# Kernel optimization log

Hardware: AMD Instinct MI355X
Metric: run time of the kernel (lower is better)

The kernel has to match this reference:

```python
import jax, jax.numpy as jnp
import numpy as np

NUM_AGENT = 200
LOOK_BACK = 10
NUM_CTRL = 9
DIM = 512
HEADS = 8
DIM_HEAD = 64
N = NUM_AGENT * LOOK_BACK + NUM_CTRL  # 2009
BATCH = 4
SCALE = DIM_HEAD ** -0.5


def _build_mask():
    # eye(num_agent) repeat_interleaved by look_back on rows and cols == kron with ones(lb,lb)
    m = jnp.kron(jnp.eye(NUM_AGENT, dtype=jnp.float32),
                 jnp.ones((LOOK_BACK, LOOK_BACK), jnp.float32))
    # pad with zeros for the control-feature rows/cols
    return jnp.pad(m, ((0, NUM_CTRL), (0, NUM_CTRL)))  # [N, N]


def _split_heads(t):
    b, n, hd = t.shape
    return t.reshape(b, n, HEADS, hd // HEADS).transpose(0, 2, 1, 3)  # [b,h,n,d]


def setup_inputs() -> dict:
    key = jax.random.key(0)
    ks = jax.random.split(key, 5)
    inner = HEADS * DIM_HEAD
    return {
        "x": jax.random.normal(ks[0], (BATCH, N, DIM), jnp.float32),
        "w_qkv": jax.random.normal(ks[1], (DIM, inner * 3), jnp.float32) * 0.02,
        "w_qk_self": jax.random.normal(ks[2], (DIM, inner * 2), jnp.float32) * 0.02,
        "w_out": jax.random.normal(ks[3], (inner, DIM), jnp.float32) * 0.02,
        "b_out": jnp.zeros((DIM,), jnp.float32),
    }


def reference(x, w_qkv, w_qk_self, w_out, b_out):
    mask = _build_mask()  # [N, N], broadcasts over [b, h]
    q, k, v = map(_split_heads, jnp.split(x @ w_qkv, 3, axis=-1))
    q_s, k_s = map(_split_heads, jnp.split(x @ w_qk_self, 2, axis=-1))
    dots = jnp.einsum('bhnd,bhmd->bhnm', q, k) * SCALE
    dots_self = jnp.einsum('bhnd,bhmd->bhnm', q_s, k_s) * SCALE
    blended = mask * dots_self + (1.0 - mask) * dots
    attn = jax.nn.softmax(blended, axis=-1)  # [b,h,n,n]
    out = jnp.einsum('bhnm,bhmd->bhnd', attn, v)
    out = out.transpose(0, 2, 1, 3).reshape(x.shape[0], N, HEADS * DIM_HEAD)
    return out @ w_out + b_out, attn
```

## Files before the change

kernel.cpp:

```cpp
#include <hip/hip_runtime.h>
#include <hip/hip_bf16.h>


#define N_TOK   2009
#define NPAD    2048
#define NTILES  16
#define NT2     32
#define BATCH_  4
#define HEADS_  8
#define MROWS   8036
#define SCALE_  0.125f
#define RPB_A   256
#define RPV     128
#define PFP     68

typedef __attribute__((ext_vector_type(8)))  short sh8;
typedef __attribute__((ext_vector_type(16))) float f32x16;

static inline int cdiv(int a, int b) { return (a + b - 1) / b; }

__device__ __forceinline__ float4 ld4(const float* p) {
    return *reinterpret_cast<const float4*>(p);
}
__device__ __forceinline__ unsigned short f2bf(float f) {
    __hip_bfloat16 h = __float2bfloat16(f);
    return *reinterpret_cast<unsigned short*>(&h);
}
__device__ __forceinline__ float bf2f(unsigned short u) {
    return __uint_as_float(((unsigned)u) << 16);
}
__device__ __forceinline__ void cvt8(const float4& a, const float4& b, sh8& hi, sh8& lo) {
    float f[8] = {a.x, a.y, a.z, a.w, b.x, b.y, b.z, b.w};
#pragma unroll
    for (int i = 0; i < 8; ++i) {
        unsigned short h = f2bf(f[i]);
        hi[i] = (short)h;
        lo[i] = (short)f2bf(f[i] - bf2f(h));
    }
}
__device__ __forceinline__ void cvt8p(const float4& a, const float4& b, sh8& hi) {
#pragma unroll
    for (int i = 0; i < 4; ++i) {
        hi[i]     = (short)f2bf((&a.x)[i]);
        hi[4 + i] = (short)f2bf((&b.x)[i]);
    }
}
typedef const __attribute__((address_space(1))) void gas_void;
typedef __attribute__((address_space(3))) void las_void;
__device__ __forceinline__ void gll16(const void* g, void* l) {
    __builtin_amdgcn_global_load_lds((gas_void*)g, (las_void*)l, 16, 0, 0);
}

__global__ __launch_bounds__(256)
void convert_x(const float* __restrict__ x, unsigned short* __restrict__ xh,
               unsigned short* __restrict__ xl)
{
    const int mt = blockIdx.x;
    const int w  = threadIdx.x >> 6;
    const int kc = threadIdx.x & 63;
    for (int it = 0; it < 8; ++it) {
        int rg = it * 4 + w;
        sh8 hi[4], lo[4];
#pragma unroll
        for (int rr = 0; rr < 4; ++rr) {
            int row = rg * 4 + rr;
            int gm = mt * 128 + row;
            int b = gm >> 11, gr = gm & 2047;
            float4 a = make_float4(0.f, 0.f, 0.f, 0.f), c = a;
            if (gr < N_TOK) {
                const float* p = x + ((size_t)b * N_TOK + gr) * 512 + kc * 8;
                a = ld4(p); c = ld4(p + 4);
            }
            cvt8(a, c, hi[rr], lo[rr]);
        }
        size_t base = ((size_t)(mt * 64 + kc) * 128 + rg * 4) * 8;
#pragma unroll
        for (int rr = 0; rr < 4; ++rr) {
            *reinterpret_cast<sh8*>(xh + base + rr * 8) = hi[rr];
            *reinterpret_cast<sh8*>(xl + base + rr * 8) = lo[rr];
        }
    }
}

__global__ __launch_bounds__(256)
void convert_w(const float* __restrict__ wqkv, const float* __restrict__ wself,
               const float* __restrict__ wout,
               unsigned short* __restrict__ qh, unsigned short* __restrict__ ql,
               unsigned short* __restrict__ sh, unsigned short* __restrict__ sl,
               unsigned short* __restrict__ oh, unsigned short* __restrict__ ol)
{
    int cid = blockIdx.x * 256 + threadIdx.x;
    int nt_all = cid >> 13, rem = cid & 8191;
    int kc = rem >> 7, col = rem & 127;
    const float* src; unsigned short *dh, *dl; int Nn, ntl;
    if (nt_all < 12)      { src = wqkv;  dh = qh; dl = ql; Nn = 1536; ntl = nt_all; }
    else if (nt_all < 20) { src = wself; dh = sh; dl = sl; Nn = 1024; ntl = nt_all - 12; }
    else                  { src = wout;  dh = oh; dl = ol; Nn = 512;  ntl = nt_all - 20; }
    float f[8];
#pragma unroll
    for (int i = 0; i < 8; ++i)
        f[i] = src[(size_t)(kc * 8 + i) * Nn + ntl * 128 + col];
    sh8 hi, lo;
    cvt8(make_float4(f[0], f[1], f[2], f[3]), make_float4(f[4], f[5], f[6], f[7]), hi, lo);
    size_t off = ((size_t)(ntl * 64 + kc) * 128 + col) * 8;
    *reinterpret_cast<sh8*>(dh + off) = hi;
    *reinterpret_cast<sh8*>(dl + off) = lo;
}

template<int MODE>
__global__ __launch_bounds__(512)
void gemm_bf16(const unsigned short* __restrict__ Ah, const unsigned short* __restrict__ Al,
               const unsigned short* __restrict__ Bh, const unsigned short* __restrict__ Bl,
               float* __restrict__ C, const float* __restrict__ bias)
{
    __shared__ __align__(16) unsigned short AhS[2][4096], AlS[2][4096],
                                            BhS[2][4096], BlS[2][4096];
    const int tid = threadIdx.x, lane = tid & 63, wid = tid >> 6;
    const int mt = blockIdx.x, ntile = blockIdx.y;
    const int wm = wid >> 2, wn = wid & 3;
    const int lj = lane & 31, g = lane >> 5;

    const unsigned short* Asrc_h = Ah + (size_t)mt * 65536;
    const unsigned short* Asrc_l = Al + (size_t)mt * 65536;
    const unsigned short* Bsrc_h = Bh + (size_t)ntile * 65536;
    const unsigned short* Bsrc_l = Bl + (size_t)ntile * 65536;

#define GSTAGE(BUF, S) do {                                                      \
    gll16(Asrc_h + (size_t)(S) * 4096 + tid * 8, (char*)AhS[BUF] + tid * 16);    \
    gll16(Asrc_l + (size_t)(S) * 4096 + tid * 8, (char*)AlS[BUF] + tid * 16);    \
    gll16(Bsrc_h + (size_t)(S) * 4096 + tid * 8, (char*)BhS[BUF] + tid * 16);    \
    gll16(Bsrc_l + (size_t)(S) * 4096 + tid * 8, (char*)BlS[BUF] + tid * 16);    \
} while (0)

    f32x16 acc[2];
#pragma unroll
    for (int i = 0; i < 16; ++i) { acc[0][i] = 0.f; acc[1][i] = 0.f; }

    GSTAGE(0, 0);
    for (int s = 0; s < 16; ++s) {
        const int buf = s & 1;
        __syncthreads();
        if (s + 1 < 16) GSTAGE(buf ^ 1, s + 1);
#pragma unroll
        for (int ks = 0; ks < 2; ++ks) {
            const int kcl = 2 * ks + g;
            sh8 bh = *reinterpret_cast<const sh8*>(BhS[buf] + (kcl * 128 + wn * 32 + lj) * 8);
            sh8 bl = *reinterpret_cast<const sh8*>(BlS[buf] + (kcl * 128 + wn * 32 + lj) * 8);
#pragma unroll
            for (int Mt = 0; Mt < 2; ++Mt) {
                sh8 ah = *reinterpret_cast<const sh8*>(AhS[buf] + (kcl * 128 + wm * 64 + Mt * 32 + lj) * 8);
                sh8 al = *reinterpret_cast<const sh8*>(AlS[buf] + (kcl * 128 + wm * 64 + Mt * 32 + lj) * 8);
                acc[Mt] = __builtin_amdgcn_mfma_f32_32x32x16_bf16(ah, bh, acc[Mt], 0, 0, 0);
                acc[Mt] = __builtin_amdgcn_mfma_f32_32x32x16_bf16(ah, bl, acc[Mt], 0, 0, 0);
                acc[Mt] = __builtin_amdgcn_mfma_f32_32x32x16_bf16(al, bh, acc[Mt], 0, 0, 0);
            }
        }
    }
#undef GSTAGE

#pragma unroll
    for (int Mt = 0; Mt < 2; ++Mt) {
#pragma unroll
        for (int reg = 0; reg < 16; ++reg) {
            int rloc = wm * 64 + Mt * 32 + (reg & 3) + 8 * (reg >> 2) + 4 * g;
            int gm = mt * 128 + rloc;
            int b = gm >> 11, gr = gm & 2047;
            if (gr < N_TOK) {
                int coln = ntile * 128 + wn * 32 + lj;
                float v = acc[Mt][reg];
                size_t idx;
                if (MODE == 1)
                    idx = ((size_t)(coln >> 9) * MROWS + (size_t)b * N_TOK + gr) * 512 + (coln & 511);
                else if (MODE == 0)
                    idx = ((size_t)b * N_TOK + gr) * 1024 + coln;
                else {
                    v += bias[coln];
                    idx = ((size_t)b * N_TOK + gr) * 512 + coln;
                }
                C[idx] = v;
            }
        }
    }
}

__global__ __launch_bounds__(256)
void selfE_k(const float* __restrict__ proj2, float* __restrict__ selfE)
{
    __shared__ float qs[10][64];
    __shared__ float ks[10][68];
    const int a = blockIdx.x;
    const int h = blockIdx.y & 7;
    const int b = blockIdx.y >> 3;
    const size_t rowbase = (size_t)b * N_TOK + a * 10;

    for (int i = threadIdx.x; i < 320; i += 256) {
        int r = i >> 4;
        int c = (i & 15) * 4;
        const float* src = proj2 + (rowbase + (r % 10)) * 1024
                         + (r < 10 ? 0 : 512) + h * 64 + c;
        float4 v = ld4(src);
        if (r < 10) *reinterpret_cast<float4*>(&qs[r][c]) = v;
        else        *reinterpret_cast<float4*>(&ks[r - 10][c]) = v;
    }
    __syncthreads();
    if (threadIdx.x < 100) {
        int r = threadIdx.x / 10, c = threadIdx.x % 10;
        float acc = 0.f;
#pragma unroll 8
        for (int d = 0; d < 64; ++d) acc += qs[r][d] * ks[c][d];
        int bh = b * HEADS_ + h;
        selfE[((size_t)bh * 2000 + a * 10 + r) * 10 + c] = __expf(acc * SCALE_);
    }
}

__global__ __launch_bounds__(256)
void convert_kv(const float* __restrict__ Kf, const float* __restrict__ Vf,
                unsigned short* __restrict__ Khg, unsigned short* __restrict__ Klg,
                unsigned short* __restrict__ Vtg)
{
    __shared__ float vtile[128][66];
    const int t  = blockIdx.x;
    const int h  = blockIdx.y & 7;
    const int b  = blockIdx.y >> 3;
    const int bh = blockIdx.y;
    const size_t bN = (size_t)b * N_TOK;
    const size_t tbase = ((size_t)bh * NTILES + t) * 8192;
    const int tid = threadIdx.x;

    {
        int r = tid >> 1, q = tid & 1;
        int gj = t * 128 + r;
        float4 f[8];
        if (gj < N_TOK) {
            const float* kp = Kf + (bN + gj) * 512 + h * 64 + q * 32;
#pragma unroll
            for (int i = 0; i < 8; ++i) f[i] = ld4(kp + 4 * i);
        } else {
#pragma unroll
            for (int i = 0; i < 8; ++i) f[i] = make_float4(0.f, 0.f, 0.f, 0.f);
        }
#pragma unroll
        for (int cp = 0; cp < 4; ++cp) {
            sh8 hi, lo;
            cvt8(f[2 * cp], f[2 * cp + 1], hi, lo);
            int kc = q * 4 + cp;
            size_t off = tbase + ((size_t)kc * 128 + r) * 8;
            *reinterpret_cast<sh8*>(Khg + off) = hi;
            *reinterpret_cast<sh8*>(Klg + off) = lo;
        }
    }
    {
        int r = tid >> 1, q = tid & 1;
        int gj = t * 128 + r;
        const float* vp = Vf + (bN + gj) * 512 + h * 64 + q * 32;
#pragma unroll
        for (int i = 0; i < 8; ++i) {
            float4 v = (gj < N_TOK) ? ld4(vp + 4 * i) : make_float4(0.f, 0.f, 0.f, 0.f);
            *reinterpret_cast<float4*>(&vtile[r][q * 32 + 4 * i]) = v;
        }
    }
    __syncthreads();
    {
        int d = tid & 63, jg = tid >> 6;
#pragma unroll
        for (int jj = 0; jj < 4; ++jj) {
            int jc = jg * 4 + jj;
            sh8 pk;
#pragma unroll
            for (int i = 0; i < 8; ++i) pk[i] = (short)f2bf(vtile[jc * 8 + i][d]);
            *reinterpret_cast<sh8*>(Vtg + tbase + ((size_t)jc * 64 + d) * 8) = pk;
        }
    }
}

__global__ __launch_bounds__(512, 2)
void attn_rowsum(const float* __restrict__ Qf,
                 const unsigned short* __restrict__ Khg,
                 const float* __restrict__ selfE,
                 float* __restrict__ rowinv)
{
    __shared__ __align__(16) unsigned short KhS[2][8192];
    __shared__ float selfS[RPB_A * 10];

    const int bid = blockIdx.x;
    const int xcd = bid & 7, idx = bid >> 3;
    const int bh  = xcd * 4 + (idx >> 3);
    const int bx  = idx & 7;
    const int h = bh & 7, b = bh >> 3;
    const int tid = threadIdx.x, lane = tid & 63, wid = tid >> 6;
    const int row0 = bx * RPB_A;
    const int wr = wid * 32;
    const size_t bN = (size_t)b * N_TOK;
    const int lj = lane & 31, g = lane >> 5;

    for (int i = tid; i < RPB_A * 10; i += 512) {
        int r = i / 10, c = i - r * 10;
        int gr = row0 + r;
        selfS[i] = (gr < 2000) ? selfE[((size_t)bh * 2000 + gr) * 10 + c] : 0.f;
    }

    sh8 qh[4];
    {
        int grow = row0 + wr + lj;
        bool val = grow < N_TOK;
        const float* qp = Qf + (bN + (val ? grow : 0)) * 512 + h * 64;
#pragma unroll
        for (int ks = 0; ks < 4; ++ks) {
            int kc = 2 * ks + g;
            float4 a = val ? ld4(qp + kc * 8)     : make_float4(0.f, 0.f, 0.f, 0.f);
            float4 c = val ? ld4(qp + kc * 8 + 4) : make_float4(0.f, 0.f, 0.f, 0.f);
            cvt8p(a, c, qh[ks]);
        }
    }

    const unsigned short* ktiles = Khg + (size_t)bh * NTILES * 8192;
#define RSTAGE(T) do {                                                          \
    const unsigned short* kt = ktiles + (size_t)(T) * 8192;                     \
    char* dst = (char*)KhS[(T) & 1];                                            \
    _Pragma("unroll") for (int i = 0; i < 2; ++i)                               \
        gll16(kt + i * 4096 + tid * 8, dst + i * 8192 + tid * 16); } while (0)

    RSTAGE(0);

    float rsacc[16];
#pragma unroll
    for (int i = 0; i < 16; ++i) rsacc[i] = 0.f;

    const int alo = (row0 / 10) * 10;
    const int rmax = row0 + RPB_A - 1 < 1999 ? row0 + RPB_A - 1 : 1999;
    const int ahi = (rmax / 10) * 10 + 10;

    for (int t = 0; t < NTILES; ++t) {
        __syncthreads();
        if (t + 1 < NTILES) RSTAGE(t + 1);
        const unsigned short* kb = KhS[t & 1];
        const bool dtile = (alo < t * 128 + 128) && (ahi > t * 128);
#pragma unroll
        for (int ct = 0; ct < 4; ++ct) {
            sh8 kf[4];
#pragma unroll
            for (int ks = 0; ks < 4; ++ks)
                kf[ks] = *reinterpret_cast<const sh8*>(kb + ((2 * ks + g) * 128 + 32 * ct + lj) * 8);
            f32x16 s;
#pragma unroll
            for (int i = 0; i < 16; ++i) s[i] = 0.f;
#pragma unroll
            for (int ks = 0; ks < 4; ++ks)
                s = __builtin_amdgcn_mfma_f32_32x32x16_bf16(qh[ks], kf[ks], s, 0, 0, 0);
            const int gj = t * 128 + 32 * ct + lj;
            if (gj < N_TOK) {
#pragma unroll
                for (int reg = 0; reg < 16; ++reg) {
                    int rloc = wr + (reg & 3) + 8 * (reg >> 2) + 4 * g;
                    int grow = row0 + rloc;
                    float e = __expf(s[reg] * SCALE_);
                    if (dtile && grow < 2000) {
                        int a0 = (grow / 10) * 10;
                        unsigned cc = (unsigned)(gj - a0);
                        if (cc < 10u) e = selfS[rloc * 10 + (int)cc];
                    }
                    rsacc[reg] += e;
                }
            }
        }
    }
#undef RSTAGE

#pragma unroll
    for (int reg = 0; reg < 16; ++reg) {
        float v = rsacc[reg];
        v += __shfl_xor(v, 1);  v += __shfl_xor(v, 2);
        v += __shfl_xor(v, 4);  v += __shfl_xor(v, 8);
        v += __shfl_xor(v, 16);
        rsacc[reg] = v;
    }
    if (lj == 0) {
#pragma unroll
        for (int reg = 0; reg < 16; ++reg) {
            int rloc = wr + (reg & 3) + 8 * (reg >> 2) + 4 * g;
            int grow = row0 + rloc;
            rowinv[(size_t)bh * NPAD + row0 + rloc] =
                (grow < N_TOK) ? 1.0f / rsacc[reg] : 0.f;
        }
    }
}

__global__ __launch_bounds__(512, 2)
void attn_pv(const float* __restrict__ Qf,
             const unsigned short* __restrict__ Khg,
             const unsigned short* __restrict__ Klg,
             const unsigned short* __restrict__ Vtg,
             const float* __restrict__ selfE,
             const float* __restrict__ rowinv,
             float* __restrict__ attn,
             unsigned short* __restrict__ Ohg, unsigned short* __restrict__ Olg)
{
    extern __shared__ __align__(16) char smem[];
    unsigned short* KhS = (unsigned short*)smem;
    unsigned short* KlS = KhS + 4096;
    unsigned short* VtS = KlS + 4096;
    float* Pf = (float*)(VtS + 8192);
    unsigned short* selfS = (unsigned short*)(Pf + RPV * PFP);
    float* rinvS = (float*)(selfS + RPV * 10);

    const int bid = blockIdx.x;
    const int xcd = bid & 7, idx = bid >> 3;
    const int bh  = xcd * 4 + (idx >> 4);
    const int bx  = idx & 15;
    const int h = bh & 7, b = bh >> 3;
    const int tid = threadIdx.x, lane = tid & 63, wid = tid >> 6;
    const int row0 = bx * RPV;
    const int wr = (wid & 3) * 32;
    const int cw = wid >> 2;
    const size_t bN = (size_t)b * N_TOK;
    const size_t abase = ((size_t)bh * N_TOK + row0) * N_TOK;
    const int lj = lane & 31, g = lane >> 5;

    for (int i = tid; i < RPV * 10; i += 512) {
        int r = i / 10, c = i - r * 10;
        int gr = row0 + r;
        selfS[i] = (gr < 2000) ? f2bf(selfE[((size_t)bh * 2000 + gr) * 10 + c]) : 0;
    }
    if (tid < RPV) rinvS[tid] = rowinv[(size_t)bh * NPAD + row0 + tid];

    sh8 qh[4], ql[4];
    {
        int grow = row0 + wr + lj;
        bool val = grow < N_TOK;
        const float* qp = Qf + (bN + (val ? grow : 0)) * 512 + h * 64;
#pragma unroll
        for (int ks = 0; ks < 4; ++ks) {
            int kc = 2 * ks + g;
            float4 a = val ? ld4(qp + kc * 8)     : make_float4(0.f, 0.f, 0.f, 0.f);
            float4 c = val ? ld4(qp + kc * 8 + 4) : make_float4(0.f, 0.f, 0.f, 0.f);
            cvt8(a, c, qh[ks], ql[ks]);
        }
    }

    const unsigned short* khT = Khg + (size_t)bh * NTILES * 8192;
    const unsigned short* klT = Klg + (size_t)bh * NTILES * 8192;
    const unsigned short* vtT = Vtg + (size_t)bh * NTILES * 8192;

#define STAGE_KH(T) gll16(khT + (size_t)((T) >> 1) * 8192                           \
        + ((size_t)(tid >> 6) * 128 + 64 * ((T) & 1) + (tid & 63)) * 8,             \
        (char*)KhS + tid * 16)
#define STAGE_KL(T) gll16(klT + (size_t)((T) >> 1) * 8192                           \
        + ((size_t)(tid >> 6) * 128 + 64 * ((T) & 1) + (tid & 63)) * 8,             \
        (char*)KlS + tid * 16)
#define STAGE_VT(T) gll16(vtT + (size_t)((T) >> 1) * 8192                           \
        + ((size_t)(8 * ((T) & 1) + (tid >> 6)) * 64 + (tid & 63)) * 8,             \
        (char*)(VtS + ((T) & 1) * 4096) + tid * 16)

    STAGE_KH(0); STAGE_KL(0); STAGE_VT(0);

    const int alo = (row0 / 10) * 10;
    const int rmax = row0 + RPV - 1 < 1999 ? row0 + RPV - 1 : 1999;
    const int ahi = (rmax / 10) * 10 + 10;

    f32x16 oacc;
#pragma unroll
    for (int i = 0; i < 16; ++i) oacc[i] = 0.f;

    __syncthreads();

    for (int t = 0; t < NT2; ++t) {
        const bool dtile = (alo < t * 64 + 64) && (ahi > t * 64);

        sh8 kfh[4], kfl[4];
#pragma unroll
        for (int ks = 0; ks < 4; ++ks) {
            int off = ((2 * ks + g) * 64 + 32 * cw + lj) * 8;
            kfh[ks] = *reinterpret_cast<const sh8*>(KhS + off);
            kfl[ks] = *reinterpret_cast<const sh8*>(KlS + off);
        }
        f32x16 s;
#pragma unroll
        for (int i = 0; i < 16; ++i) s[i] = 0.f;
#pragma unroll
        for (int ks = 0; ks < 4; ++ks) {
            s = __builtin_amdgcn_mfma_f32_32x32x16_bf16(qh[ks], kfh[ks], s, 0, 0, 0);
            s = __builtin_amdgcn_mfma_f32_32x32x16_bf16(qh[ks], kfl[ks], s, 0, 0, 0);
            s = __builtin_amdgcn_mfma_f32_32x32x16_bf16(ql[ks], kfh[ks], s, 0, 0, 0);
        }
        const int cin = 32 * cw + lj;
        const int gj  = t * 64 + cin;
        const bool jv = gj < N_TOK;
#pragma unroll
        for (int reg = 0; reg < 16; ++reg) {
            int rowl = (reg & 3) + 8 * (reg >> 2) + 4 * g;
            int rloc = wr + rowl;
            int grow = row0 + rloc;
            float e = 0.f;
            if (jv && grow < N_TOK) e = __expf(s[reg] * SCALE_);
            if (dtile && jv && grow < 2000) {
                int a0 = (grow / 10) * 10;
                unsigned cc = (unsigned)(gj - a0);
                if (cc < 10u) e = bf2f(selfS[rloc * 10 + (int)cc]);
            }
            Pf[rloc * PFP + cin] = e * rinvS[rloc];
        }
        __syncthreads();

        if (t + 1 < NT2) { STAGE_KH(t + 1); STAGE_KL(t + 1); STAGE_VT(t + 1); }
        const unsigned short* vtb = VtS + (t & 1) * 4096;
#pragma unroll
        for (int m = 0; m < 4; ++m) {
            const float* pp = &Pf[(wr + lj) * PFP + 16 * m + 8 * g];
            float4 a = ld4(pp), b4 = ld4(pp + 4);
            sh8 pa; cvt8p(a, b4, pa);
            sh8 vf = *reinterpret_cast<const sh8*>(vtb + ((2 * m + g) * 64 + 32 * cw + lj) * 8);
            oacc = __builtin_amdgcn_mfma_f32_32x32x16_bf16(pa, vf, oacc, 0, 0, 0);
        }
        {
            const int c4  = (tid & 15) * 4;
            const int gj0 = t * 64 + c4;
#pragma unroll
            for (int it = 0; it < 4; ++it) {
                int r = it * 32 + (tid >> 4);
                int grow = row0 + r;
                if (grow < N_TOK) {
                    float4 v = ld4(&Pf[r * PFP + c4]);
                    float* ap = attn + abase + (size_t)r * N_TOK + gj0;
                    if (gj0 + 3 < N_TOK) {
                        *reinterpret_cast<float4*>(ap) = v;
                    } else {
#pragma unroll
                        for (int e = 0; e < 4; ++e)
                            if (gj0 + e < N_TOK) ap[e] = (&v.x)[e];
                    }
                }
            }
        }
        __syncthreads();
    }
#undef STAGE_KH
#undef STAGE_KL
#undef STAGE_VT

    float* Ofull = (float*)smem;
#pragma unroll
    for (int reg = 0; reg < 16; ++reg) {
        int rloc = wr + (reg & 3) + 8 * (reg >> 2) + 4 * g;
        Ofull[rloc * 68 + 32 * cw + lj] = oacc[reg];
    }
    __syncthreads();
#pragma unroll
    for (int it = 0; it < 2; ++it) {
        int task = it * 512 + tid;
        int row = task >> 3, kq = task & 7;
        const float* op = Ofull + row * 68 + kq * 8;
        float4 a = ld4(op), c = ld4(op + 4);
        sh8 hi, lo; cvt8(a, c, hi, lo);
        int gm = b * 2048 + row0 + row;
        int mtile = gm >> 7, row128 = gm & 127;
        size_t off = ((size_t)(mtile * 64 + h * 8 + kq) * 128 + row128) * 8;
        *reinterpret_cast<sh8*>(Ohg + off) = hi;
        *reinterpret_cast<sh8*>(Olg + off) = lo;
    }
}

extern "C" void kernel_launch(void* const* d_in, const int* in_sizes, int n_in,
                              void* d_out, int out_size, void* d_ws, size_t ws_size,
                              hipStream_t stream)
{
    const float* x         = (const float*)d_in[0];
    const float* w_qkv     = (const float*)d_in[1];
    const float* w_qk_self = (const float*)d_in[2];
    const float* w_out     = (const float*)d_in[3];
    const float* b_out     = (const float*)d_in[4];

    float* out  = (float*)d_out;
    float* attn = out + (size_t)MROWS * 512;

    float* Qf = (float*)d_ws;
    float* Kf = Qf + (size_t)MROWS * 512;
    float* Vf = Kf + (size_t)MROWS * 512;
    float* p2 = Vf + (size_t)MROWS * 512;
    unsigned short* Khg = (unsigned short*)p2;
    unsigned short* Klg = Khg + 4194304;
    unsigned short* Vtg = Klg + 4194304;
    float* proj2 = p2;
    float* after_p2 = p2 + (size_t)MROWS * 1024;
    unsigned short* xh  = (unsigned short*)after_p2;
    unsigned short* xl  = xh + 4194304;
    unsigned short* Wqh = xl + 4194304;
    unsigned short* Wql = Wqh + 786432;
    unsigned short* Wsh = Wql + 786432;
    unsigned short* Wsl = Wsh + 524288;
    unsigned short* Woh = Wsl + 524288;
    unsigned short* Wol = Woh + 262144;
    float* rowinv = (float*)(Wol + 262144);
    float* selfE  = rowinv + 65536;
    unsigned short* Ohg = (unsigned short*)Kf;
    unsigned short* Olg = Ohg + 4194304;

    const int smem_pv = 8192 + 8192 + 16384
                      + RPV * PFP * 4
                      + RPV * 10 * 2 + RPV * 4;
    hipFuncSetAttribute((const void*)attn_pv,
                        hipFuncAttributeMaxDynamicSharedMemorySize, smem_pv);

    convert_x<<<64, 256, 0, stream>>>(x, xh, xl);
    convert_w<<<768, 256, 0, stream>>>(w_qkv, w_qk_self, w_out,
                                       Wqh, Wql, Wsh, Wsl, Woh, Wol);

    dim3 g1(64, 12);
    gemm_bf16<1><<<g1, 512, 0, stream>>>(xh, xl, Wqh, Wql, Qf, nullptr);

    dim3 g2(64, 8);
    gemm_bf16<0><<<g2, 512, 0, stream>>>(xh, xl, Wsh, Wsl, proj2, nullptr);

    dim3 gs(200, 32);
    selfE_k<<<gs, 256, 0, stream>>>(proj2, selfE);

    dim3 gc(NTILES, 32);
    convert_kv<<<gc, 256, 0, stream>>>(Kf, Vf, Khg, Klg, Vtg);

    attn_rowsum<<<256, 512, 0, stream>>>(Qf, Khg, selfE, rowinv);

    attn_pv<<<512, 512, smem_pv, stream>>>(Qf, Khg, Klg, Vtg, selfE, rowinv,
                                           attn, Ohg, Olg);

    dim3 g3(64, 4);
    gemm_bf16<2><<<g3, 512, 0, stream>>>(Ohg, Olg, Woh, Wol, out, b_out);
}
```

Baseline: 460.0 us.

## Relax attn_pv barriers so attention stores overlap the next tile's loads

Splits the attn_pv tile loop into QK and PV phase macros and peels off the last iteration. Each __syncthreads is replaced by a hand-written barrier: one waits only on LDS, and the other waits with vmcnt(4), so the four attention-row stores can stay in flight while the prefetched K/V loads are still required to land. The stores are made branch-free by sending invalid rows to a scratch dump buffer, which keeps the outstanding-store count fixed. The aim is to stop draining all global stores at every tile barrier. The cost is reliance on exact vmcnt ordering and an extra scratch region carved from the workspace.

```diff
diff --git a/kernel.cpp b/kernel.cpp
--- a/kernel.cpp
+++ b/kernel.cpp
@@ -49,6 +49,19 @@
 typedef __attribute__((address_space(3))) void las_void;
 __device__ __forceinline__ void gll16(const void* g, void* l) {
     __builtin_amdgcn_global_load_lds((gas_void*)g, (las_void*)l, 16, 0, 0);
+}
+
+__device__ __forceinline__ void bar_lds() {
+    asm volatile("s_waitcnt lgkmcnt(0)" ::: "memory");
+    __builtin_amdgcn_sched_barrier(0);
+    __builtin_amdgcn_s_barrier();
+    __builtin_amdgcn_sched_barrier(0);
+}
+__device__ __forceinline__ void bar_keep4() {
+    asm volatile("s_waitcnt vmcnt(4) lgkmcnt(0)" ::: "memory");
+    __builtin_amdgcn_sched_barrier(0);
+    __builtin_amdgcn_s_barrier();
+    __builtin_amdgcn_sched_barrier(0);
 }
 
 __global__ __launch_bounds__(256)
@@ -393,7 +406,8 @@
              const float* __restrict__ selfE,
              const float* __restrict__ rowinv,
              float* __restrict__ attn,
-             unsigned short* __restrict__ Ohg, unsigned short* __restrict__ Olg)
+             unsigned short* __restrict__ Ohg, unsigned short* __restrict__ Olg,
+             float* __restrict__ dump)
 {
     extern __shared__ __align__(16) char smem[];
     unsigned short* KhS = (unsigned short*)smem;
@@ -415,6 +429,7 @@
     const size_t bN = (size_t)b * N_TOK;
     const size_t abase = ((size_t)bh * N_TOK + row0) * N_TOK;
     const int lj = lane & 31, g = lane >> 5;
+    float* dumpT = dump + ((size_t)bh * 512 + tid) * 4;
 
     for (int i = tid; i < RPV * 10; i += 512) {
         int r = i / 10, c = i - r * 10;
@@ -451,6 +466,51 @@
         + ((size_t)(8 * ((T) & 1) + (tid >> 6)) * 64 + (tid & 63)) * 8,             \
         (char*)(VtS + ((T) & 1) * 4096) + tid * 16)
 
+#define QK_PHASE(T) do {                                                            \
+        const bool dtile = (alo < (T) * 64 + 64) && (ahi > (T) * 64);               \
+        sh8 kfh[4], kfl[4];                                                         \
+        _Pragma("unroll") for (int ks = 0; ks < 4; ++ks) {                          \
+            int off = ((2 * ks + g) * 64 + 32 * cw + lj) * 8;                       \
+            kfh[ks] = *reinterpret_cast<const sh8*>(KhS + off);                     \
+            kfl[ks] = *reinterpret_cast<const sh8*>(KlS + off);                     \
+        }                                                                           \
+        f32x16 s;                                                                   \
+        _Pragma("unroll") for (int i = 0; i < 16; ++i) s[i] = 0.f;                  \
+        _Pragma("unroll") for (int ks = 0; ks < 4; ++ks) {                          \
+            s = __builtin_amdgcn_mfma_f32_32x32x16_bf16(qh[ks], kfh[ks], s, 0,0,0); \
+            s = __builtin_amdgcn_mfma_f32_32x32x16_bf16(qh[ks], kfl[ks], s, 0,0,0); \
+            s = __builtin_amdgcn_mfma_f32_32x32x16_bf16(ql[ks], kfh[ks], s, 0,0,0); \
+        }                                                                           \
+        const int cin = 32 * cw + lj;                                               \
+        const int gj  = (T) * 64 + cin;                                             \
+        const bool jv = gj < N_TOK;                                                 \
+        _Pragma("unroll") for (int reg = 0; reg < 16; ++reg) {                      \
+            int rowl = (reg & 3) + 8 * (reg >> 2) + 4 * g;                          \
+            int rloc = wr + rowl;                                                   \
+            int grow = row0 + rloc;                                                 \
+            float e = 0.f;                                                          \
+            if (jv && grow < N_TOK) e = __expf(s[reg] * SCALE_);                    \
+            if (dtile && jv && grow < 2000) {                                       \
+                int a0 = (grow / 10) * 10;                                          \
+                unsigned cc = (unsigned)(gj - a0);                                  \
+                if (cc < 10u) e = bf2f(selfS[rloc * 10 + (int)cc]);                 \
+            }                                                                       \
+            Pf[rloc * PFP + cin] = e * rinvS[rloc];                                 \
+        }                                                                           \
+    } while (0)
+
+#define PV_PHASE(T) do {                                                            \
+        const unsigned short* vtb = VtS + ((T) & 1) * 4096;                         \
+        _Pragma("unroll") for (int m = 0; m < 4; ++m) {                             \
+            const float* pp = &Pf[(wr + lj) * PFP + 16 * m + 8 * g];                \
+            float4 a = ld4(pp), b4 = ld4(pp + 4);                                   \
+            sh8 pa; cvt8p(a, b4, pa);                                               \
+            sh8 vf = *reinterpret_cast<const sh8*>(                                 \
+                vtb + ((2 * m + g) * 64 + 32 * cw + lj) * 8);                       \
+            oacc = __builtin_amdgcn_mfma_f32_32x32x16_bf16(pa, vf, oacc, 0, 0, 0);  \
+        }                                                                           \
+    } while (0)
+
     STAGE_KH(0); STAGE_KL(0); STAGE_VT(0);
 
     const int alo = (row0 / 10) * 10;
@@ -463,54 +523,32 @@
 
     __syncthreads();
 
-    for (int t = 0; t < NT2; ++t) {
-        const bool dtile = (alo < t * 64 + 64) && (ahi > t * 64);
-
-        sh8 kfh[4], kfl[4];
-#pragma unroll
-        for (int ks = 0; ks < 4; ++ks) {
-            int off = ((2 * ks + g) * 64 + 32 * cw + lj) * 8;
-            kfh[ks] = *reinterpret_cast<const sh8*>(KhS + off);
-            kfl[ks] = *reinterpret_cast<const sh8*>(KlS + off);
-        }
-        f32x16 s;
-#pragma unroll
-        for (int i = 0; i < 16; ++i) s[i] = 0.f;
-#pragma unroll
-        for (int ks = 0; ks < 4; ++ks) {
-            s = __builtin_amdgcn_mfma_f32_32x32x16_bf16(qh[ks], kfh[ks], s, 0, 0, 0);
-            s = __builtin_amdgcn_mfma_f32_32x32x16_bf16(qh[ks], kfl[ks], s, 0, 0, 0);
-            s = __builtin_amdgcn_mfma_f32_32x32x16_bf16(ql[ks], kfh[ks], s, 0, 0, 0);
-        }
-        const int cin = 32 * cw + lj;
-        const int gj  = t * 64 + cin;
-        const bool jv = gj < N_TOK;
-#pragma unroll
-        for (int reg = 0; reg < 16; ++reg) {
-            int rowl = (reg & 3) + 8 * (reg >> 2) + 4 * g;
-            int rloc = wr + rowl;
-            int grow = row0 + rloc;
-            float e = 0.f;
-            if (jv && grow < N_TOK) e = __expf(s[reg] * SCALE_);
-            if (dtile && jv && grow < 2000) {
-                int a0 = (grow / 10) * 10;
-                unsigned cc = (unsigned)(gj - a0);
-                if (cc < 10u) e = bf2f(selfS[rloc * 10 + (int)cc]);
+    for (int t = 0; t < NT2 - 1; ++t) {
+        QK_PHASE(t);
+        bar_lds();
+        STAGE_KH(t + 1); STAGE_KL(t + 1); STAGE_VT(t + 1);
+        {
+            const int c4  = (tid & 15) * 4;
+            const int gj0 = t * 64 + c4;
+#pragma unroll
+            for (int it = 0; it < 4; ++it) {
+                int r = it * 32 + (tid >> 4);
+                int grow = row0 + r;
+                float4 v = ld4(&Pf[r * PFP + c4]);
+                float* ap = attn + abase + (size_t)r * N_TOK + gj0;
+                float* sdst = (grow < N_TOK) ? ap : dumpT;
+                *reinterpret_cast<float4*>(sdst) = v;
             }
-            Pf[rloc * PFP + cin] = e * rinvS[rloc];
-        }
+        }
+        PV_PHASE(t);
+        bar_keep4();
+    }
+
+    {
+        const int t = NT2 - 1;
+        QK_PHASE(t);
         __syncthreads();
-
-        if (t + 1 < NT2) { STAGE_KH(t + 1); STAGE_KL(t + 1); STAGE_VT(t + 1); }
-        const unsigned short* vtb = VtS + (t & 1) * 4096;
-#pragma unroll
-        for (int m = 0; m < 4; ++m) {
-            const float* pp = &Pf[(wr + lj) * PFP + 16 * m + 8 * g];
-            float4 a = ld4(pp), b4 = ld4(pp + 4);
-            sh8 pa; cvt8p(a, b4, pa);
-            sh8 vf = *reinterpret_cast<const sh8*>(vtb + ((2 * m + g) * 64 + 32 * cw + lj) * 8);
-            oacc = __builtin_amdgcn_mfma_f32_32x32x16_bf16(pa, vf, oacc, 0, 0, 0);
-        }
+        PV_PHASE(t);
         {
             const int c4  = (tid & 15) * 4;
             const int gj0 = t * 64 + c4;
@@ -536,6 +574,8 @@
 #undef STAGE_KH
 #undef STAGE_KL
 #undef STAGE_VT
+#undef QK_PHASE
+#undef PV_PHASE
 
     float* Ofull = (float*)smem;
 #pragma unroll
@@ -591,6 +631,7 @@
     unsigned short* Wol = Woh + 262144;
     float* rowinv = (float*)(Wol + 262144);
     float* selfE  = rowinv + 65536;
+    float* dump   = selfE + 640000;
     unsigned short* Ohg = (unsigned short*)Kf;
     unsigned short* Olg = Ohg + 4194304;
 
@@ -619,7 +660,7 @@
     attn_rowsum<<<256, 512, 0, stream>>>(Qf, Khg, selfE, rowinv);
 
     attn_pv<<<512, 512, smem_pv, stream>>>(Qf, Khg, Klg, Vtg, selfE, rowinv,
-                                           attn, Ohg, Olg);
+                                           attn, Ohg, Olg, dump);
 
     dim3 g3(64, 4);
     gemm_bf16<2><<<g3, 512, 0, stream>>>(Ohg, Olg, Woh, Wol, out, b_out);
```

Result: slower. 474.2 us (+3.1%).
